# Performance work log

Measured on AMD Instinct MI355X. Metric: run time of the kernel, lower is better.

Reference implementation:

```python
import jax, jax.numpy as jnp
import numpy as np

SEQ_LEN = 128
IN_F = 16
OUT_F = 16
K_ORDER = 3
BATCH = 1024


def setup_inputs() -> dict:
    key = jax.random.key(0)
    k1, k2, k3 = jax.random.split(key, 3)
    x = jax.random.normal(k1, (BATCH, SEQ_LEN, IN_F), dtype=jnp.float32)
    # Glorot-uniform init for weight [k, in, out]
    lim = float(np.sqrt(6.0 / (IN_F + OUT_F)))
    weight = jax.random.uniform(k2, (K_ORDER, IN_F, OUT_F), dtype=jnp.float32, minval=-lim, maxval=lim)
    bias = jnp.zeros((OUT_F,), dtype=jnp.float32)
    adj_param = jax.random.normal(k3, (IN_F, IN_F), dtype=jnp.float32)
    return {"x": x, "weight": weight, "bias": bias, "adj_param": adj_param}


def _cheb_polynomials(adj_param, seq_len, in_f, k_order):
    """Vectorized build of the normalized-Laplacian Chebyshev basis.

    Replaces the original per-element Python loops:
      - temporal edges: node (i,f) <-> (i+1,f)  (symmetric shift by in_f)
      - feature edges : sigmoid(adj_param) off-diagonal, block-diag per time step
    """
    n = seq_len * in_f
    eye_n = jnp.eye(n, dtype=jnp.float32)
    # temporal edges
    offs = jnp.arange((seq_len - 1) * in_f)
    temporal = jnp.zeros((n, n), dtype=jnp.float32).at[offs, offs + in_f].set(1.0)
    temporal = temporal + temporal.T
    # feature edges (zero diagonal), replicated block-diagonally over time
    feat = jax.nn.sigmoid(adj_param) * (1.0 - jnp.eye(in_f, dtype=jnp.float32))
    adj = temporal + jnp.kron(jnp.eye(seq_len, dtype=jnp.float32), feat) + eye_n
    # symmetric normalization: L = I - D^{-1/2} A D^{-1/2}
    d = jnp.sum(adj, axis=1)
    d_inv_sqrt = jnp.where(d > 0, d ** -0.5, 0.0)
    lap = eye_n - d_inv_sqrt[:, None] * adj * d_inv_sqrt[None, :]
    # spectral rescale: L_scaled = 2/||L||_2 * L - I  (||.||_2 = largest singular value)
    l_scaled = (2.0 / jnp.linalg.norm(lap, ord=2)) * lap - eye_n
    polys = [eye_n, l_scaled]
    for _ in range(2, k_order):
        polys.append(2.0 * (l_scaled @ polys[-1]) - polys[-2])
    return polys


def reference(x, weight, bias, adj_param):
    batch, seq_len, in_f = x.shape
    k_order, _, out_f = weight.shape
    polys = _cheb_polynomials(adj_param, seq_len, in_f, k_order)
    x_flat = x.reshape(batch, seq_len * in_f)  # [B, N]
    out = jnp.zeros((batch, seq_len, out_f), dtype=x.dtype)
    for k in range(k_order):
        x_k = (x_flat @ polys[k]).reshape(batch, seq_len, in_f)
        out = out + jnp.einsum("bsf,fo->bso", x_k, weight[k])
    return out + bias
```

## Files before the change

kernel.cpp:

```cpp
#include <hip/hip_runtime.h>
#include <math.h>


#define MU_MIN (-1.99940694f)
#define MSTRIDE 1300

__device__ __forceinline__ float dot16(float x) {
  x += __shfl_xor(x, 1);
  x += __shfl_xor(x, 2);
  x += __shfl_xor(x, 4);
  x += __shfl_xor(x, 8);
  return x;
}

__global__ __launch_bounds__(256) void k_all(const float* __restrict__ adj,
                                             const float* __restrict__ W,
                                             const float* __restrict__ x,
                                             const float* __restrict__ bias,
                                             float* __restrict__ out) {
  const int bg = blockIdx.x;
  const int tg = blockIdx.y;
  const int t0 = tg * 16, b0 = bg * 16;
  const int tid = threadIdx.x;

  __shared__ float Bsh[256], Wsh[768];
  __shared__ float dis_i[16], dis_b[16], csh[1];
  __shared__ float H0[512], Pb[512], Qb[512];
  __shared__ float scl[2], lamsh[2];
  __shared__ int jst[2];
  __shared__ float Dint[256], Dbnd[256], DDint[256], DDbnd[256];
  __shared__ float Msh[4 * MSTRIDE];
  __shared__ float xs[1600];

  float4 xpre0, xpre1;
  {
    const int idx = tid;
    const int cb = idx / 80, rem = idx % 80;
    const int rrow = rem >> 2, qq = rem & 3;
    int gr = t0 - 2 + rrow;
    gr = gr < 0 ? 0 : (gr > 127 ? 127 : gr);
    xpre0 = *(const float4*)(x + ((size_t)(b0 + cb) * 128 + gr) * 16 + qq * 4);
  }
  if (tid < 64) {
    const int idx = tid + 256;
    const int cb = idx / 80, rem = idx % 80;
    const int rrow = rem >> 2, qq = rem & 3;
    int gr = t0 - 2 + rrow;
    gr = gr < 0 ? 0 : (gr > 127 ? 127 : gr);
    xpre1 = *(const float4*)(x + ((size_t)(b0 + cb) * 128 + gr) * 16 + qq * 4);
  }

  {
    const int f = tid >> 4, g = tid & 15;
    const float a = adj[tid];
    const float s = 1.f / (1.f + expf(-a));
    Bsh[tid] = (f == g) ? 1.f : s;
    Wsh[tid] = W[tid];
    Wsh[tid + 256] = W[tid + 256];
    Wsh[tid + 512] = W[tid + 512];
  }
  __syncthreads();
  if (tid < 16) {
    float rs = 0.f;
    #pragma unroll
    for (int j = 0; j < 16; j++) rs += Bsh[tid * 16 + j];
    dis_i[tid] = rsqrtf(rs + 2.f);
    dis_b[tid] = rsqrtf(rs + 1.f);
  }
  __syncthreads();

  const int pass = tid >> 7, idx = tid & 127;
  const int pb = pass * 256;
  const float mu = pass ? -MU_MIN : MU_MIN;
  for (int e = idx; e < 256; e += 128) {
    const int f = e >> 4, g = e & 15;
    float gv = -dis_i[f] * Bsh[e] * dis_i[g];
    if (f == g) gv += 1.f - mu * dis_i[f] * dis_i[f];
    Pb[pb + e] = gv;
  }
  __syncthreads();
  for (int e = idx; e < 256; e += 128) {
    const int r = e >> 4, q = e & 15;
    float s = 0.f;
    #pragma unroll
    for (int k = 0; k < 16; k++) s += Pb[pb + k * 16 + r] * Pb[pb + k * 16 + q];
    H0[pb + e] = s;
    Qb[pb + e] = s;
  }
  __syncthreads();
  float* cur = Qb;
  float* nxt = Pb;
  #pragma unroll 1
  for (int it = 0; it < 8; it++) {
    if (idx == 0) {
      float tr = 0.f;
      #pragma unroll
      for (int d = 0; d < 16; d++) tr += cur[pb + d * 17];
      scl[pass] = 1.f / (tr * tr);
    }
    __syncthreads();
    const float s2 = scl[pass];
    for (int e = idx; e < 256; e += 128) {
      const int r = e >> 4, q = e & 15;
      const float4* rr = (const float4*)(cur + pb + r * 16);
      const float4* qq = (const float4*)(cur + pb + q * 16);
      float s = 0.f;
      #pragma unroll
      for (int k4 = 0; k4 < 4; k4++) {
        const float4 a = rr[k4], b = qq[k4];
        s += a.x * b.x + a.y * b.y + a.z * b.z + a.w * b.w;
      }
      nxt[pb + e] = s * s2;
    }
    __syncthreads();
    float* tmp = cur; cur = nxt; nxt = tmp;
  }
  if (idx == 0) {
    int bj = 0; float bd = -1.f;
    #pragma unroll
    for (int d = 0; d < 16; d++) {
      const float v = cur[pb + d * 17];
      if (v > bd) { bd = v; bj = d; }
    }
    jst[pass] = bj;
  }
  __syncthreads();
  if (idx < 16) {
    const int r = idx, js = jst[pass];
    const float vr = cur[pb + r * 16 + js];
    float hv = 0.f;
    #pragma unroll
    for (int q = 0; q < 16; q++) hv += H0[pb + r * 16 + q] * cur[pb + q * 16 + js];
    const float num = dot16(vr * hv);
    const float den = dot16(vr * vr);
    if (r == 0) lamsh[pass] = num / fmaxf(den, 1e-30f);
  }
  __syncthreads();
  if (tid == 0) {
    const float lam = fmaxf(fmaxf(lamsh[0], lamsh[1]), 1e-20f);
    csh[0] = 2.f / sqrtf(lam);
  }
  __syncthreads();

  const float c = csh[0];
  const int r = tid >> 4, q = tid & 15;
  Dint[tid] = ((r == q) ? (c - 1.f) : 0.f) - c * dis_i[r] * dis_i[q] * Bsh[tid];
  Dbnd[tid] = ((r == q) ? (c - 1.f) : 0.f) - c * dis_b[r] * dis_b[q] * Bsh[tid];
  __syncthreads();
  {
    float s0 = 0.f, s1 = 0.f;
    #pragma unroll
    for (int k = 0; k < 16; k++) {
      s0 += Dint[r * 16 + k] * Dint[k * 16 + q];
      s1 += Dbnd[r * 16 + k] * Dbnd[k * 16 + q];
    }
    DDint[tid] = s0;
    DDbnd[tid] = s1;
  }
  __syncthreads();

  int tvs[4], nv;
  if (tg == 0)      { nv = 4; tvs[0] = 8; tvs[1] = 0;   tvs[2] = 1;   tvs[3] = 2;   }
  else if (tg == 7) { nv = 4; tvs[0] = 8; tvs[1] = 125; tvs[2] = 126; tvs[3] = 127; }
  else              { nv = 1; tvs[0] = 8; }

  const int fo = r;
  const int o = q;
  auto uat = [&](int a_, int ff) -> float {
    return (a_ == 0 || a_ == 127) ? dis_b[ff] : dis_i[ff];
  };

  #pragma unroll 1
  for (int v = 0; v < nv; v++) {
    const int t = tvs[v];
    const float* D0p = (t == 0 || t == 127) ? Dbnd : Dint;
    const float* Dmp = (t == 1)   ? Dbnd : Dint;
    const float* Dpp = (t == 126) ? Dbnd : Dint;
    const float* DDp = (t == 0 || t == 127) ? DDbnd : DDint;
    float m[5];
    const float ut_f = uat(t, fo);

    {
      float acc = Wsh[fo * 16 + o];
      const float diag0 = 2.f * c * c * ut_f * ut_f *
                          ((t > 0 ? uat(t - 1, fo) * uat(t - 1, fo) : 0.f) +
                           (t < 127 ? uat(t + 1, fo) * uat(t + 1, fo) : 0.f)) - 1.f;
      #pragma unroll
      for (int fp = 0; fp < 16; fp++) {
        acc += D0p[fo * 16 + fp] * Wsh[256 + fp * 16 + o];
        const float p2 = 2.f * DDp[fo * 16 + fp] + ((fo == fp) ? diag0 : 0.f);
        acc += p2 * Wsh[512 + fp * 16 + o];
      }
      m[2] = acc;
    }
    if (t < 127) {
      const float gf = -c * uat(t + 1, fo) * ut_f;
      float acc = gf * Wsh[256 + fo * 16 + o];
      #pragma unroll
      for (int fp = 0; fp < 16; fp++) {
        const float gq = -c * uat(t + 1, fp) * uat(t, fp);
        acc += 2.f * (gf * D0p[fo * 16 + fp] + Dpp[fo * 16 + fp] * gq) * Wsh[512 + fp * 16 + o];
      }
      m[3] = acc;
    } else m[3] = 0.f;
    if (t > 0) {
      const float gf = -c * uat(t - 1, fo) * ut_f;
      float acc = gf * Wsh[256 + fo * 16 + o];
      #pragma unroll
      for (int fp = 0; fp < 16; fp++) {
        const float gq = -c * uat(t - 1, fp) * uat(t, fp);
        acc += 2.f * (Dmp[fo * 16 + fp] * gq + gf * D0p[fo * 16 + fp]) * Wsh[512 + fp * 16 + o];
      }
      m[1] = acc;
    } else m[1] = 0.f;
    m[4] = (t < 126) ? (2.f * c * c * uat(t + 2, fo) * uat(t + 1, fo) * uat(t + 1, fo) * ut_f
                        * Wsh[512 + fo * 16 + o]) : 0.f;
    m[0] = (t > 1) ? (2.f * c * c * uat(t - 2, fo) * uat(t - 1, fo) * uat(t - 1, fo) * ut_f
                      * Wsh[512 + fo * 16 + o]) : 0.f;

    float* Mv = Msh + v * MSTRIDE;
    #pragma unroll
    for (int d5 = 0; d5 < 5; d5++)
      Mv[d5 * 256 + fo * 16 + o] = m[d5];
  }

  {
    const int cb = tid / 80, rem = tid % 80;
    const int rrow = rem >> 2, qq = rem & 3;
    *(float4*)(xs + cb * 400 + rrow * 20 + qq * 4) = xpre0;
  }
  if (tid < 64) {
    const int idx2 = tid + 256;
    const int cb = idx2 / 80, rem = idx2 % 80;
    const int rrow = rem >> 2, qq = rem & 3;
    *(float4*)(xs + cb * 400 + rrow * 20 + qq * 4) = xpre1;
  }
  __syncthreads();

  const int tl = r;
  const int t = t0 + tl;
  int vm = 0;
  if (tg == 0)      vm = (tl < 3)  ? tl + 1  : 0;
  else if (tg == 7) vm = (tl > 12) ? tl - 12 : 0;
  float M[80];
  {
    const float* Mv = Msh + vm * MSTRIDE;
    #pragma unroll
    for (int dt = 0; dt < 5; dt++)
      #pragma unroll
      for (int f = 0; f < 16; f++)
        M[dt * 16 + f] = Mv[dt * 256 + f * 16 + o];
  }
  const float bo = bias[o];

  for (int cc = 0; cc < 4; cc++) {
    if (cc > 0) {
      __syncthreads();
      for (int ix = tid; ix < 320; ix += 256) {
        const int cb = ix / 80, rem = ix % 80;
        const int rrow = rem >> 2, qq = rem & 3;
        int gr = t0 - 2 + rrow;
        gr = gr < 0 ? 0 : (gr > 127 ? 127 : gr);
        const float4 vv = *(const float4*)(x + ((size_t)(b0 + cc * 4 + cb) * 128 + gr) * 16 + qq * 4);
        *(float4*)(xs + cb * 400 + rrow * 20 + qq * 4) = vv;
      }
      __syncthreads();
    }
    #pragma unroll
    for (int cb = 0; cb < 4; cb++) {
      float acc0 = bo, acc1 = 0.f;
      #pragma unroll
      for (int dt = 0; dt < 5; dt++) {
        const float* xr = xs + cb * 400 + (tl + dt) * 20;
        const float4 xa = *(const float4*)(xr);
        const float4 xb = *(const float4*)(xr + 4);
        const float4 xc = *(const float4*)(xr + 8);
        const float4 xd = *(const float4*)(xr + 12);
        const float* Mp = M + dt * 16;
        acc0 += xa.x * Mp[0] + xa.y * Mp[1] + xa.z * Mp[2] + xa.w * Mp[3]
              + xb.x * Mp[4] + xb.y * Mp[5] + xb.z * Mp[6] + xb.w * Mp[7];
        acc1 += xc.x * Mp[8] + xc.y * Mp[9] + xc.z * Mp[10] + xc.w * Mp[11]
              + xd.x * Mp[12] + xd.y * Mp[13] + xd.z * Mp[14] + xd.w * Mp[15];
      }
      out[((size_t)(b0 + cc * 4 + cb) * 128 + t) * 16 + o] = acc0 + acc1;
    }
  }
}

extern "C" void kernel_launch(void* const* d_in, const int* in_sizes, int n_in,
                              void* d_out, int out_size, void* d_ws, size_t ws_size,
                              hipStream_t stream) {
  const float* x    = (const float*)d_in[0];
  const float* W    = (const float*)d_in[1];
  const float* bias = (const float*)d_in[2];
  const float* adj  = (const float*)d_in[3];
  float* out = (float*)d_out;
  (void)d_ws; (void)ws_size;

  k_all<<<dim3(64, 8), dim3(256), 0, stream>>>(adj, W, x, bias, out);
}
```

Measured before the change: 86.92 us.

## Double-buffer x tiles with register prefetch and fuse setup stages to cut barriers

```diff
diff --git a/kernel.cpp b/kernel.cpp
--- a/kernel.cpp
+++ b/kernel.cpp
@@ -26,24 +26,23 @@
   __shared__ float Bsh[256], Wsh[768];
   __shared__ float dis_i[16], dis_b[16], csh[1];
   __shared__ float H0[512], Pb[512], Qb[512];
-  __shared__ float scl[2], lamsh[2];
+  __shared__ float lamsh[2];
   __shared__ int jst[2];
   __shared__ float Dint[256], Dbnd[256], DDint[256], DDbnd[256];
   __shared__ float Msh[4 * MSTRIDE];
-  __shared__ float xs[1600];
+  __shared__ float xs[3200];
 
   float4 xpre0, xpre1;
   {
-    const int idx = tid;
-    const int cb = idx / 80, rem = idx % 80;
+    const int cb = tid / 80, rem = tid % 80;
     const int rrow = rem >> 2, qq = rem & 3;
     int gr = t0 - 2 + rrow;
     gr = gr < 0 ? 0 : (gr > 127 ? 127 : gr);
     xpre0 = *(const float4*)(x + ((size_t)(b0 + cb) * 128 + gr) * 16 + qq * 4);
   }
   if (tid < 64) {
-    const int idx = tid + 256;
-    const int cb = idx / 80, rem = idx % 80;
+    const int ix = tid + 256;
+    const int cb = ix / 80, rem = ix % 80;
     const int rrow = rem >> 2, qq = rem & 3;
     int gr = t0 - 2 + rrow;
     gr = gr < 0 ? 0 : (gr > 127 ? 127 : gr);
@@ -73,33 +72,31 @@
   const int pb = pass * 256;
   const float mu = pass ? -MU_MIN : MU_MIN;
   for (int e = idx; e < 256; e += 128) {
-    const int f = e >> 4, g = e & 15;
-    float gv = -dis_i[f] * Bsh[e] * dis_i[g];
-    if (f == g) gv += 1.f - mu * dis_i[f] * dis_i[f];
-    Pb[pb + e] = gv;
-  }
-  __syncthreads();
-  for (int e = idx; e < 256; e += 128) {
     const int r = e >> 4, q = e & 15;
+    const float ur = dis_i[r], uq = dis_i[q];
     float s = 0.f;
     #pragma unroll
-    for (int k = 0; k < 16; k++) s += Pb[pb + k * 16 + r] * Pb[pb + k * 16 + q];
+    for (int k = 0; k < 16; k++) {
+      const float uk = dis_i[k];
+      float gkr = -uk * Bsh[k * 16 + r] * ur;
+      if (k == r) gkr += 1.f - mu * uk * uk;
+      float gkq = -uk * Bsh[k * 16 + q] * uq;
+      if (k == q) gkq += 1.f - mu * uk * uk;
+      s += gkr * gkq;
+    }
     H0[pb + e] = s;
     Qb[pb + e] = s;
   }
   __syncthreads();
+
   float* cur = Qb;
   float* nxt = Pb;
   #pragma unroll 1
   for (int it = 0; it < 8; it++) {
-    if (idx == 0) {
-      float tr = 0.f;
-      #pragma unroll
-      for (int d = 0; d < 16; d++) tr += cur[pb + d * 17];
-      scl[pass] = 1.f / (tr * tr);
-    }
-    __syncthreads();
-    const float s2 = scl[pass];
+    float tr = 0.f;
+    #pragma unroll
+    for (int d = 0; d < 16; d++) tr += cur[pb + d * 17];
+    const float s2 = 1.f / (tr * tr);
     for (int e = idx; e < 256; e += 128) {
       const int r = e >> 4, q = e & 15;
       const float4* rr = (const float4*)(cur + pb + r * 16);
@@ -230,8 +227,8 @@
     *(float4*)(xs + cb * 400 + rrow * 20 + qq * 4) = xpre0;
   }
   if (tid < 64) {
-    const int idx2 = tid + 256;
-    const int cb = idx2 / 80, rem = idx2 % 80;
+    const int ix = tid + 256;
+    const int cb = ix / 80, rem = ix % 80;
     const int rrow = rem >> 2, qq = rem & 3;
     *(float4*)(xs + cb * 400 + rrow * 20 + qq * 4) = xpre1;
   }
@@ -254,24 +251,29 @@
   const float bo = bias[o];
 
   for (int cc = 0; cc < 4; cc++) {
-    if (cc > 0) {
-      __syncthreads();
-      for (int ix = tid; ix < 320; ix += 256) {
-        const int cb = ix / 80, rem = ix % 80;
-        const int rrow = rem >> 2, qq = rem & 3;
-        int gr = t0 - 2 + rrow;
-        gr = gr < 0 ? 0 : (gr > 127 ? 127 : gr);
-        const float4 vv = *(const float4*)(x + ((size_t)(b0 + cc * 4 + cb) * 128 + gr) * 16 + qq * 4);
-        *(float4*)(xs + cb * 400 + rrow * 20 + qq * 4) = vv;
-      }
-      __syncthreads();
+    const float* xbuf = xs + (cc & 1) * 1600;
+    float4 pre0, pre1;
+    if (cc < 3) {
+      const int cb = tid / 80, rem = tid % 80;
+      const int rrow = rem >> 2, qq = rem & 3;
+      int gr = t0 - 2 + rrow;
+      gr = gr < 0 ? 0 : (gr > 127 ? 127 : gr);
+      pre0 = *(const float4*)(x + ((size_t)(b0 + (cc + 1) * 4 + cb) * 128 + gr) * 16 + qq * 4);
+      if (tid < 64) {
+        const int ix = tid + 256;
+        const int cb2 = ix / 80, rem2 = ix % 80;
+        const int rrow2 = rem2 >> 2, qq2 = rem2 & 3;
+        int gr2 = t0 - 2 + rrow2;
+        gr2 = gr2 < 0 ? 0 : (gr2 > 127 ? 127 : gr2);
+        pre1 = *(const float4*)(x + ((size_t)(b0 + (cc + 1) * 4 + cb2) * 128 + gr2) * 16 + qq2 * 4);
+      }
     }
     #pragma unroll
     for (int cb = 0; cb < 4; cb++) {
       float acc0 = bo, acc1 = 0.f;
       #pragma unroll
       for (int dt = 0; dt < 5; dt++) {
-        const float* xr = xs + cb * 400 + (tl + dt) * 20;
+        const float* xr = xbuf + cb * 400 + (tl + dt) * 20;
         const float4 xa = *(const float4*)(xr);
         const float4 xb = *(const float4*)(xr + 4);
         const float4 xc = *(const float4*)(xr + 8);
@@ -284,6 +286,21 @@
       }
       out[((size_t)(b0 + cc * 4 + cb) * 128 + t) * 16 + o] = acc0 + acc1;
     }
+    if (cc < 3) {
+      float* nbuf = xs + ((cc + 1) & 1) * 1600;
+      {
+        const int cb = tid / 80, rem = tid % 80;
+        const int rrow = rem >> 2, qq = rem & 3;
+        *(float4*)(nbuf + cb * 400 + rrow * 20 + qq * 4) = pre0;
+      }
+      if (tid < 64) {
+        const int ix = tid + 256;
+        const int cb = ix / 80, rem = ix % 80;
+        const int rrow = rem >> 2, qq = rem & 3;
+        *(float4*)(nbuf + cb * 400 + rrow * 20 + qq * 4) = pre1;
+      }
+      __syncthreads();
+    }
   }
 }
 
```

After: 86.08 us. Within noise of the previous version (-1.0%).
